# Optimization experiments

Measured on AMD Instinct MI355X. Metric: run time of the kernel, lower is better.

Reference implementation:

```python
import jax, jax.numpy as jnp
import numpy as np

FEATS = 1024
HEAD = 16
MLP_HIDDEN = 4096
B, N = 8, 1024
EPS = 1e-5


def _layernorm(x, g, b):
    mu = jnp.mean(x, axis=-1, keepdims=True)
    var = jnp.var(x, axis=-1, keepdims=True)
    return (x - mu) * jax.lax.rsqrt(var + EPS) * g + b


def setup_inputs() -> dict:
    key = jax.random.key(0)
    ks = jax.random.split(key, 12)
    s_attn = 1.0 / np.sqrt(FEATS)
    s_mlp1 = 1.0 / np.sqrt(FEATS)
    s_mlp2 = 1.0 / np.sqrt(MLP_HIDDEN)
    return {
        "x": jax.random.normal(ks[0], (B, N, FEATS), dtype=jnp.float32),
        "ln1_g": jnp.ones((FEATS,), jnp.float32),
        "ln1_b": jnp.zeros((FEATS,), jnp.float32),
        "wq": jax.random.normal(ks[1], (FEATS, FEATS), jnp.float32) * s_attn,
        "bq": jnp.zeros((FEATS,), jnp.float32),
        "wk": jax.random.normal(ks[2], (FEATS, FEATS), jnp.float32) * s_attn,
        "bk": jnp.zeros((FEATS,), jnp.float32),
        "wv": jax.random.normal(ks[3], (FEATS, FEATS), jnp.float32) * s_attn,
        "bv": jnp.zeros((FEATS,), jnp.float32),
        "wo": jax.random.normal(ks[4], (FEATS, FEATS), jnp.float32) * s_attn,
        "bo": jnp.zeros((FEATS,), jnp.float32),
        "ln2_g": jnp.ones((FEATS,), jnp.float32),
        "ln2_b": jnp.zeros((FEATS,), jnp.float32),
        "w1": jax.random.normal(ks[5], (FEATS, MLP_HIDDEN), jnp.float32) * s_mlp1,
        "b1": jnp.zeros((MLP_HIDDEN,), jnp.float32),
        "w2": jax.random.normal(ks[6], (MLP_HIDDEN, FEATS), jnp.float32) * s_mlp2,
        "b2": jnp.zeros((FEATS,), jnp.float32),
    }


def reference(x, ln1_g, ln1_b, wq, bq, wk, bk, wv, bv, wo, bo,
              ln2_g, ln2_b, w1, b1, w2, b2):
    b, n, f = x.shape
    d = f // HEAD
    sqrt_d = jnp.asarray(f, x.dtype) ** 0.5  # NOTE: scale by sqrt(feats), as in source

    h = _layernorm(x, ln1_g, ln1_b)
    # [b, n, f] -> [b, head, n, d]
    q = (h @ wq + bq).reshape(b, n, HEAD, d).transpose(0, 2, 1, 3)
    k = (h @ wk + bk).reshape(b, n, HEAD, d).transpose(0, 2, 1, 3)
    v = (h @ wv + bv).reshape(b, n, HEAD, d).transpose(0, 2, 1, 3)

    score = jnp.einsum('bhif,bhjf->bhij', q, k) / sqrt_d
    p = jax.nn.softmax(score, axis=-1)
    attn = jnp.einsum('bhij,bhjf->bihf', p, v).reshape(b, n, f)
    o = attn @ wo + bo
    out = o + x

    h2 = _layernorm(out, ln2_g, ln2_b)
    m = jax.nn.gelu(h2 @ w1 + b1, approximate=False)
    m = jax.nn.gelu(m @ w2 + b2, approximate=False)
    return m + out
```

## Files before the change

kernel.cpp:

```cpp
#include <hip/hip_runtime.h>
#include <cstdint>

typedef __bf16 bf16;
typedef __attribute__((ext_vector_type(8))) __bf16 bf16x8;
typedef __attribute__((ext_vector_type(4))) __bf16 bf16x4;
typedef __attribute__((ext_vector_type(4))) float f32x4;
typedef __attribute__((ext_vector_type(8))) unsigned short u16x8;

#define AS1C(p) ((const __attribute__((address_space(1))) void*)(p))
#define AS3(p)  ((__attribute__((address_space(3))) void*)(p))

__device__ __forceinline__ float gelu_exact(float v) {
    return 0.5f * v * (1.0f + erff(v * 0.7071067811865476f));
}

__global__ __launch_bounds__(256, 1) void wtrans_kernel(
    const float* __restrict__ w, bf16* __restrict__ wt, int K, int N)
{
    __shared__ float tile[64][65];
    const int k0 = blockIdx.y * 64, n0 = blockIdx.x * 64;
    const int tid = threadIdx.x;
    {
        const int kl = tid >> 2, nc = (tid & 3) * 16;
        #pragma unroll
        for (int i = 0; i < 4; ++i) {
            const float4 v = *(const float4*)&w[(size_t)(k0 + kl) * N + n0 + nc + i * 4];
            tile[kl][nc + i * 4 + 0] = v.x;
            tile[kl][nc + i * 4 + 1] = v.y;
            tile[kl][nc + i * 4 + 2] = v.z;
            tile[kl][nc + i * 4 + 3] = v.w;
        }
    }
    __syncthreads();
    {
        const int nl = tid >> 2, kc = (tid & 3) * 16;
        #pragma unroll
        for (int i = 0; i < 4; ++i) {
            bf16x4 o4;
            o4[0] = (bf16)tile[kc + i * 4 + 0][nl];
            o4[1] = (bf16)tile[kc + i * 4 + 1][nl];
            o4[2] = (bf16)tile[kc + i * 4 + 2][nl];
            o4[3] = (bf16)tile[kc + i * 4 + 3][nl];
            *(bf16x4*)&wt[(size_t)(n0 + nl) * K + k0 + kc + i * 4] = o4;
        }
    }
}

__global__ void bias3_kernel(const float* __restrict__ a, const float* __restrict__ b,
                             const float* __restrict__ c, float* __restrict__ o)
{
    const int i = blockIdx.x * 256 + threadIdx.x;
    o[i] = (i < 1024) ? a[i] : (i < 2048 ? b[i - 1024] : c[i - 2048]);
}

__global__ __launch_bounds__(256, 1) void ln_kernel(
    const float* __restrict__ x, const float* __restrict__ gw,
    const float* __restrict__ bw, bf16* __restrict__ out)
{
    const int row = blockIdx.x, tid = threadIdx.x;
    const float4 v = *(const float4*)&x[(size_t)row * 1024 + tid * 4];
    float s = v.x + v.y + v.z + v.w;
    float q = v.x * v.x + v.y * v.y + v.z * v.z + v.w * v.w;
    #pragma unroll
    for (int off = 32; off > 0; off >>= 1) {
        s += __shfl_xor(s, off);
        q += __shfl_xor(q, off);
    }
    __shared__ float red[8];
    if ((tid & 63) == 0) { red[tid >> 6] = s; red[4 + (tid >> 6)] = q; }
    __syncthreads();
    s = red[0] + red[1] + red[2] + red[3];
    q = red[4] + red[5] + red[6] + red[7];
    const float mu = s * (1.f / 1024.f);
    const float rs = rsqrtf(q * (1.f / 1024.f) - mu * mu + 1e-5f);
    const float4 gg = *(const float4*)&gw[tid * 4];
    const float4 bb = *(const float4*)&bw[tid * 4];
    bf16x4 o4;
    o4[0] = (bf16)((v.x - mu) * rs * gg.x + bb.x);
    o4[1] = (bf16)((v.y - mu) * rs * gg.y + bb.y);
    o4[2] = (bf16)((v.z - mu) * rs * gg.z + bb.z);
    o4[3] = (bf16)((v.w - mu) * rs * gg.w + bb.w);
    *(bf16x4*)&out[(size_t)row * 1024 + tid * 4] = o4;
}

template<int EPI>
__global__ __launch_bounds__(512, 2) void gemm_v7_kernel(
    const bf16* __restrict__ A, const bf16* __restrict__ BT,
    const float* __restrict__ bias, const float* __restrict__ res,
    void* __restrict__ out, int M, int N, int K)
{
    constexpr int ABYTES = 256 * 128;
    constexpr int BUFB = 384 * 128;
    extern __shared__ char lds[];

    const int tid = threadIdx.x;
    const int lane = tid & 63, wid = tid >> 6;
    const int wr = wid >> 1, wc = wid & 1;
    const int j = lane & 15, g = lane >> 4;
    const int skc = ((tid & 7) ^ ((tid >> 4) & 7)) << 3;

    const int nbn = N >> 7;
    const int nwg = (M >> 8) * nbn;
    const int bid = blockIdx.x;
    const int wg = (bid & 7) * (nwg >> 3) + (bid >> 3);
    const int bm = (wg / nbn) << 8;
    const int bn = (wg % nbn) << 7;

    auto stage = [&](int k0, char* obuf) {
        #pragma unroll
        for (int ga = 0; ga < 4; ++ga) {
            const bf16* src = A + (size_t)(bm + ga * 64 + (tid >> 3)) * K + k0 + skc;
            __builtin_amdgcn_global_load_lds(AS1C(src), AS3(obuf + ga * 8192 + tid * 16), 16, 0, 0);
        }
        #pragma unroll
        for (int gb = 0; gb < 2; ++gb) {
            const bf16* src = BT + (size_t)(bn + gb * 64 + (tid >> 3)) * K + k0 + skc;
            __builtin_amdgcn_global_load_lds(AS1C(src), AS3(obuf + ABYTES + gb * 8192 + tid * 16), 16, 0, 0);
        }
    };

    f32x4 acc[4][4] = {};
    const int NT = K >> 6;

    stage(0, lds);
    stage(64, lds + BUFB);
    asm volatile("s_waitcnt vmcnt(6)" ::: "memory");
    __builtin_amdgcn_s_barrier();

    int cur = 0;
    for (int t = 0; t < NT; ++t) {
        char* buf = lds + cur * BUFB;
        const int nxt2 = (cur >= 1) ? cur - 1 : 2;

        bf16x8 af[4][2], bfr[2][2];
        #pragma unroll
        for (int mf = 0; mf < 4; ++mf)
            #pragma unroll
            for (int ks = 0; ks < 2; ++ks) {
                const int R = wr * 64 + mf * 16 + j;
                uint32_t lb = (uint32_t)(R * 128 + ks * 64 + g * 16);
                lb ^= (lb >> 4) & 0x70u;
                af[mf][ks] = *(const bf16x8*)(buf + lb);
            }
        #pragma unroll
        for (int nf = 0; nf < 2; ++nf)
            #pragma unroll
            for (int ks = 0; ks < 2; ++ks) {
                const int R = wc * 64 + nf * 16 + j;
                uint32_t lb = (uint32_t)(R * 128 + ks * 64 + g * 16);
                lb ^= (lb >> 4) & 0x70u;
                bfr[nf][ks] = *(const bf16x8*)(buf + ABYTES + lb);
            }
        if (t + 2 < NT) stage((t + 2) << 6, lds + nxt2 * BUFB);
        __builtin_amdgcn_s_barrier();
        asm volatile("s_waitcnt lgkmcnt(0)" ::: "memory");
        __builtin_amdgcn_sched_barrier(0);
        __builtin_amdgcn_s_setprio(1);
        #pragma unroll
        for (int mf = 0; mf < 4; ++mf)
            #pragma unroll
            for (int nf = 0; nf < 2; ++nf)
                #pragma unroll
                for (int ks = 0; ks < 2; ++ks)
                    acc[mf][nf] = __builtin_amdgcn_mfma_f32_16x16x32_bf16(
                        af[mf][ks], bfr[nf][ks], acc[mf][nf], 0, 0, 0);
        __builtin_amdgcn_s_setprio(0);
        __builtin_amdgcn_s_barrier();

        bf16x8 bfr2[2][2];
        #pragma unroll
        for (int nf = 0; nf < 2; ++nf)
            #pragma unroll
            for (int ks = 0; ks < 2; ++ks) {
                const int R = wc * 64 + (2 + nf) * 16 + j;
                uint32_t lb = (uint32_t)(R * 128 + ks * 64 + g * 16);
                lb ^= (lb >> 4) & 0x70u;
                bfr2[nf][ks] = *(const bf16x8*)(buf + ABYTES + lb);
            }
        __builtin_amdgcn_s_barrier();
        asm volatile("s_waitcnt lgkmcnt(0)" ::: "memory");
        __builtin_amdgcn_sched_barrier(0);
        __builtin_amdgcn_s_setprio(1);
        #pragma unroll
        for (int mf = 0; mf < 4; ++mf)
            #pragma unroll
            for (int nf = 0; nf < 2; ++nf)
                #pragma unroll
                for (int ks = 0; ks < 2; ++ks)
                    acc[mf][2 + nf] = __builtin_amdgcn_mfma_f32_16x16x32_bf16(
                        af[mf][ks], bfr2[nf][ks], acc[mf][2 + nf], 0, 0, 0);
        __builtin_amdgcn_s_setprio(0);
        if (t + 2 < NT) asm volatile("s_waitcnt vmcnt(6)" ::: "memory");
        else            asm volatile("s_waitcnt vmcnt(0)" ::: "memory");
        __builtin_amdgcn_s_barrier();

        cur = (cur == 2) ? 0 : cur + 1;
    }

    const int row0 = bm + wr * 64;
    const int col0 = bn + wc * 64;
    #pragma unroll
    for (int nf = 0; nf < 4; ++nf) {
        const int col = col0 + nf * 16 + j;
        const float bs = bias[col];
        #pragma unroll
        for (int mf = 0; mf < 4; ++mf) {
            #pragma unroll
            for (int r = 0; r < 4; ++r) {
                const int row = row0 + mf * 16 + g * 4 + r;
                float v = acc[mf][nf][r] + bs;
                if constexpr (EPI == 2 || EPI == 3) v = gelu_exact(v);
                if constexpr (EPI == 1 || EPI == 3) {
                    v += res[(size_t)row * N + col];
                    ((float*)out)[(size_t)row * N + col] = v;
                } else {
                    ((bf16*)out)[(size_t)row * N + col] = (bf16)v;
                }
            }
        }
    }
}

__global__ __launch_bounds__(256, 1) void attn_kernel(
    const bf16* __restrict__ qkv, bf16* __restrict__ attn, int bh_base)
{
    const int tid = threadIdx.x;
    const int lane = tid & 63, wid = tid >> 6;
    const int j = lane & 15, g = lane >> 4;

    const int lin = blockIdx.x + blockIdx.y * 8;
    const int virt = (lin & 7) * 64 + (lin >> 3);
    const int bh = bh_base + (virt >> 3), qp = virt & 7;
    const int b = bh >> 4, h = bh & 15;
    const int q0a = qp * 128 + wid * 16;
    const int q0b = q0a + 64;

    const bf16* Qp = qkv + (size_t)b * 1024 * 3072 + h * 64;
    const bf16* Kp = Qp + 1024;
    const bf16* Vp = Qp + 2048;

    __shared__ __attribute__((aligned(16))) uint32_t vTu[4][64][36];

    const int kp = (tid & 31) * 2;
    const int d0 = (tid >> 5) * 8;
    #pragma unroll
    for (int pb = 0; pb < 2; ++pb) {
        const u16x8 r0 = *(const u16x8*)&Vp[(size_t)(pb * 64 + kp) * 3072 + d0];
        const u16x8 r1 = *(const u16x8*)&Vp[(size_t)(pb * 64 + kp + 1) * 3072 + d0];
        #pragma unroll
        for (int i = 0; i < 8; ++i)
            vTu[pb][d0 + i][kp >> 1] = (uint32_t)r0[i] | ((uint32_t)r1[i] << 16);
    }

    bf16x8 qa0 = *(const bf16x8*)&Qp[(size_t)(q0a + j) * 3072 + g * 8];
    bf16x8 qa1 = *(const bf16x8*)&Qp[(size_t)(q0a + j) * 3072 + 32 + g * 8];
    bf16x8 qb0 = *(const bf16x8*)&Qp[(size_t)(q0b + j) * 3072 + g * 8];
    bf16x8 qb1 = *(const bf16x8*)&Qp[(size_t)(q0b + j) * 3072 + 32 + g * 8];
    #pragma unroll
    for (int e = 0; e < 8; ++e) {
        qa0[e] = (bf16)((float)qa0[e] * 0.03125f);
        qa1[e] = (bf16)((float)qa1[e] * 0.03125f);
        qb0[e] = (bf16)((float)qb0[e] * 0.03125f);
        qb1[e] = (bf16)((float)qb1[e] * 0.03125f);
    }

    const int jperm = (j >> 2) * 8 + (j & 3);

    f32x4 oa[4] = {}, ob[4] = {};
    float mra = -1e30f, lsa = 0.f;
    float mrb = -1e30f, lsb = 0.f;

    bf16x8 kfA[4][2], kfB[4][2];
    #pragma unroll
    for (int t = 0; t < 4; ++t) {
        const int key = (t >> 1) * 32 + jperm + (t & 1) * 4;
        kfA[t][0] = *(const bf16x8*)&Kp[(size_t)key * 3072 + g * 8];
        kfA[t][1] = *(const bf16x8*)&Kp[(size_t)key * 3072 + 32 + g * 8];
    }

    asm volatile("s_waitcnt lgkmcnt(0)" ::: "memory");
    __builtin_amdgcn_s_barrier();

    auto softmax = [&](f32x4 (&s)[4], float& mrun, float& lsum, f32x4 (&o)[4]) {
        float cur = fmaxf(fmaxf(s[0][0], s[0][1]), fmaxf(s[0][2], s[0][3]));
        #pragma unroll
        for (int t = 1; t < 4; ++t)
            cur = fmaxf(cur, fmaxf(fmaxf(s[t][0], s[t][1]), fmaxf(s[t][2], s[t][3])));
        cur = fmaxf(cur, __shfl_xor(cur, 16));
        cur = fmaxf(cur, __shfl_xor(cur, 32));
        if (!__all(cur - mrun <= 8.0f)) {
            const float mnew = fmaxf(mrun, cur);
            const float alpha = __expf(mrun - mnew);
            float al[4];
            #pragma unroll
            for (int r = 0; r < 4; ++r) al[r] = __shfl(alpha, g * 4 + r);
            #pragma unroll
            for (int dt = 0; dt < 4; ++dt)
                #pragma unroll
                for (int r = 0; r < 4; ++r) o[dt][r] *= al[r];
            lsum *= alpha;
            mrun = mnew;
        }
        float ps = 0.f;
        #pragma unroll
        for (int t = 0; t < 4; ++t)
            #pragma unroll
            for (int r = 0; r < 4; ++r) {
                const float p = __expf(s[t][r] - mrun);
                s[t][r] = p;
                ps += p;
            }
        lsum += ps;
    };

    auto iter = [&](int c, bf16x8 (&kf)[4][2], bf16x8 (&kfn)[4][2]) {
        const f32x4 zero = {0.f, 0.f, 0.f, 0.f};
        const bool pfv = (c + 2 < 16);
        const bool pfk = (c + 1 < 16);

        u16x8 r0, r1;
        if (pfv) {
            const size_t vb = (size_t)((c + 2) * 64 + kp) * 3072 + d0;
            r0 = *(const u16x8*)&Vp[vb];
            r1 = *(const u16x8*)&Vp[vb + 3072];
        }

        f32x4 sa[4], sb[4];
        #pragma unroll
        for (int t = 0; t < 4; ++t) {
            sa[t] = __builtin_amdgcn_mfma_f32_16x16x32_bf16(kf[t][0], qa0, zero, 0, 0, 0);
            sb[t] = __builtin_amdgcn_mfma_f32_16x16x32_bf16(kf[t][0], qb0, zero, 0, 0, 0);
            sa[t] = __builtin_amdgcn_mfma_f32_16x16x32_bf16(kf[t][1], qa1, sa[t], 0, 0, 0);
            sb[t] = __builtin_amdgcn_mfma_f32_16x16x32_bf16(kf[t][1], qb1, sb[t], 0, 0, 0);
        }

        if (pfk) {
            #pragma unroll
            for (int t = 0; t < 4; ++t) {
                const int key = (c + 1) * 64 + (t >> 1) * 32 + jperm + (t & 1) * 4;
                kfn[t][0] = *(const bf16x8*)&Kp[(size_t)key * 3072 + g * 8];
                kfn[t][1] = *(const bf16x8*)&Kp[(size_t)key * 3072 + 32 + g * 8];
            }
        }

        softmax(sa, mra, lsa, oa);
        softmax(sb, mrb, lsb, ob);

        bf16x8 paa0, paa1, pab0, pab1;
        #pragma unroll
        for (int r = 0; r < 4; ++r) {
            paa0[r]     = (bf16)sa[0][r];
            paa0[4 + r] = (bf16)sa[1][r];
            paa1[r]     = (bf16)sa[2][r];
            paa1[4 + r] = (bf16)sa[3][r];
            pab0[r]     = (bf16)sb[0][r];
            pab0[4 + r] = (bf16)sb[1][r];
            pab1[r]     = (bf16)sb[2][r];
            pab1[4 + r] = (bf16)sb[3][r];
        }

        if (pfv) {
            const int wb = (c + 2) & 3;
            #pragma unroll
            for (int i = 0; i < 8; ++i)
                vTu[wb][d0 + i][kp >> 1] = (uint32_t)r0[i] | ((uint32_t)r1[i] << 16);
        }

        const int rb = c & 3;
        #pragma unroll
        for (int dt = 0; dt < 4; ++dt) {
            const bf16* vrow = (const bf16*)&vTu[rb][dt * 16 + j][0];
            const bf16x8 vb0 = *(const bf16x8*)(vrow + g * 8);
            const bf16x8 vb1 = *(const bf16x8*)(vrow + 32 + g * 8);
            oa[dt] = __builtin_amdgcn_mfma_f32_16x16x32_bf16(paa0, vb0, oa[dt], 0, 0, 0);
            ob[dt] = __builtin_amdgcn_mfma_f32_16x16x32_bf16(pab0, vb0, ob[dt], 0, 0, 0);
            oa[dt] = __builtin_amdgcn_mfma_f32_16x16x32_bf16(paa1, vb1, oa[dt], 0, 0, 0);
            ob[dt] = __builtin_amdgcn_mfma_f32_16x16x32_bf16(pab1, vb1, ob[dt], 0, 0, 0);
        }
    };

    for (int cc = 0; cc < 16; cc += 2) {
        iter(cc,     kfA, kfB);
        iter(cc + 1, kfB, kfA);
        asm volatile("s_waitcnt lgkmcnt(0)" ::: "memory");
        __builtin_amdgcn_sched_barrier(0);
        __builtin_amdgcn_s_barrier();
    }

    lsa += __shfl_xor(lsa, 16);
    lsa += __shfl_xor(lsa, 32);
    lsb += __shfl_xor(lsb, 16);
    lsb += __shfl_xor(lsb, 32);
    float inva[4], invb[4];
    #pragma unroll
    for (int r = 0; r < 4; ++r) {
        inva[r] = 1.0f / __shfl(lsa, g * 4 + r);
        invb[r] = 1.0f / __shfl(lsb, g * 4 + r);
    }
    #pragma unroll
    for (int dt = 0; dt < 4; ++dt)
        #pragma unroll
        for (int r = 0; r < 4; ++r) {
            attn[(size_t)(b * 1024 + q0a + g * 4 + r) * 1024 + h * 64 + dt * 16 + j] =
                (bf16)(oa[dt][r] * inva[r]);
            attn[(size_t)(b * 1024 + q0b + g * 4 + r) * 1024 + h * 64 + dt * 16 + j] =
                (bf16)(ob[dt][r] * invb[r]);
        }
}

extern "C" void kernel_launch(void* const* d_in, const int* in_sizes, int n_in,
                              void* d_out, int out_size, void* d_ws, size_t ws_size,
                              hipStream_t stream)
{
    const float* x    = (const float*)d_in[0];
    const float* ln1g = (const float*)d_in[1];
    const float* ln1b = (const float*)d_in[2];
    const float* wq   = (const float*)d_in[3];
    const float* bq   = (const float*)d_in[4];
    const float* wk   = (const float*)d_in[5];
    const float* bk   = (const float*)d_in[6];
    const float* wv   = (const float*)d_in[7];
    const float* bv   = (const float*)d_in[8];
    const float* wo   = (const float*)d_in[9];
    const float* bo   = (const float*)d_in[10];
    const float* ln2g = (const float*)d_in[11];
    const float* ln2b = (const float*)d_in[12];
    const float* w1   = (const float*)d_in[13];
    const float* b1   = (const float*)d_in[14];
    const float* w2   = (const float*)d_in[15];
    const float* b2   = (const float*)d_in[16];

    char* ws = (char*)d_ws;
    bf16* wqkvT = (bf16*)ws;  ws += (size_t)3072 * 1024 * 2;
    bf16* woT   = (bf16*)ws;  ws += (size_t)1024 * 1024 * 2;
    bf16* w1T   = (bf16*)ws;  ws += (size_t)4096 * 1024 * 2;
    bf16* w2T   = (bf16*)ws;  ws += (size_t)1024 * 4096 * 2;
    float* bqkv = (float*)ws; ws += (size_t)3072 * 4;
    bf16* h     = (bf16*)ws;  ws += (size_t)8192 * 1024 * 2;
    bf16* qkv   = (bf16*)ws;  ws += (size_t)8192 * 3072 * 2;
    bf16* attn  = (bf16*)ws;  ws += (size_t)8192 * 1024 * 2;
    float* outf = (float*)ws; ws += (size_t)8192 * 1024 * 4;
    bf16* m1    = (bf16*)ws;  ws += (size_t)8192 * 4096 * 2;

    (void)hipFuncSetAttribute((const void*)gemm_v7_kernel<0>,
                              hipFuncAttributeMaxDynamicSharedMemorySize, 147456);
    (void)hipFuncSetAttribute((const void*)gemm_v7_kernel<1>,
                              hipFuncAttributeMaxDynamicSharedMemorySize, 147456);
    (void)hipFuncSetAttribute((const void*)gemm_v7_kernel<2>,
                              hipFuncAttributeMaxDynamicSharedMemorySize, 147456);
    (void)hipFuncSetAttribute((const void*)gemm_v7_kernel<3>,
                              hipFuncAttributeMaxDynamicSharedMemorySize, 147456);

    wtrans_kernel<<<dim3(16, 16), 256, 0, stream>>>(wq, wqkvT,                   1024, 1024);
    wtrans_kernel<<<dim3(16, 16), 256, 0, stream>>>(wk, wqkvT + 1024 * 1024,     1024, 1024);
    wtrans_kernel<<<dim3(16, 16), 256, 0, stream>>>(wv, wqkvT + 2 * 1024 * 1024, 1024, 1024);
    wtrans_kernel<<<dim3(16, 16), 256, 0, stream>>>(wo, woT, 1024, 1024);
    wtrans_kernel<<<dim3(64, 16), 256, 0, stream>>>(w1, w1T, 1024, 4096);
    wtrans_kernel<<<dim3(16, 64), 256, 0, stream>>>(w2, w2T, 4096, 1024);
    bias3_kernel<<<12, 256, 0, stream>>>(bq, bk, bv, bqkv);

    ln_kernel<<<8192, 256, 0, stream>>>(x, ln1g, ln1b, h);
    gemm_v7_kernel<0><<<768, 512, 147456, stream>>>(h, wqkvT, bqkv, nullptr, qkv, 8192, 3072, 1024);
    attn_kernel<<<dim3(8, 64), 256, 0, stream>>>(qkv, attn, 0);
    attn_kernel<<<dim3(8, 64), 256, 0, stream>>>(qkv, attn, 64);
    gemm_v7_kernel<1><<<256, 512, 147456, stream>>>(attn, woT, bo, x, outf, 8192, 1024, 1024);
    ln_kernel<<<8192, 256, 0, stream>>>(outf, ln2g, ln2b, h);
    gemm_v7_kernel<2><<<1024, 512, 147456, stream>>>(h, w1T, b1, nullptr, m1, 8192, 4096, 1024);
    gemm_v7_kernel<3><<<256, 512, 147456, stream>>>(m1, w2T, b2, outf, (float*)d_out, 8192, 1024, 4096);
}
```

Before: 449.9 us.

## Enlarge GEMM tiles to 256x256, double-buffer, and split-K the final MLP GEMM

The GEMM moves from 256x128 tiles with a three-stage buffer to 256x256 tiles with a two-stage double buffer. Each wave now computes a 128x64 sub-tile, which raises MFMA work per LDS read. The down-projection GEMM is split in two along K, writing fp32 partial sums, and a new reduce kernel adds them with bias, GELU and the residual. Larger tiles halve the number of workgroups, so the grid may underfill the CUs. The shallower pipeline and full vmcnt(0) waits expose more memory latency, and split-K adds extra fp32 traffic.

```diff
diff --git a/kernel.cpp b/kernel.cpp
--- a/kernel.cpp
+++ b/kernel.cpp
@@ -84,133 +84,135 @@
 }
 
 template<int EPI>
-__global__ __launch_bounds__(512, 2) void gemm_v7_kernel(
+__global__ __launch_bounds__(512, 2) void gemm_v10_kernel(
     const bf16* __restrict__ A, const bf16* __restrict__ BT,
     const float* __restrict__ bias, const float* __restrict__ res,
-    void* __restrict__ out, int M, int N, int K)
+    void* __restrict__ out, int M, int N, int Kstride, int Klen)
 {
     constexpr int ABYTES = 256 * 128;
-    constexpr int BUFB = 384 * 128;
+    constexpr int BUFB = 512 * 128;
     extern __shared__ char lds[];
 
     const int tid = threadIdx.x;
     const int lane = tid & 63, wid = tid >> 6;
-    const int wr = wid >> 1, wc = wid & 1;
+    const int wr = wid >> 2, wc = wid & 3;
     const int j = lane & 15, g = lane >> 4;
     const int skc = ((tid & 7) ^ ((tid >> 4) & 7)) << 3;
 
-    const int nbn = N >> 7;
+    const int nbn = N >> 8;
     const int nwg = (M >> 8) * nbn;
-    const int bid = blockIdx.x;
-    const int wg = (bid & 7) * (nwg >> 3) + (bid >> 3);
-    const int bm = (wg / nbn) << 8;
-    const int bn = (wg % nbn) << 7;
-
-    auto stage = [&](int k0, char* obuf) {
+    const int wg = (blockIdx.x & 7) * ((int)gridDim.x >> 3) + (blockIdx.x >> 3);
+    const int half = wg / nwg;
+    const int wgl = wg - half * nwg;
+    const int bm = (wgl / nbn) << 8;
+    const int bn = (wgl % nbn) << 8;
+    const int kbase = half * Klen;
+
+    const bf16* srcA[4];
+    const bf16* srcB[4];
+    #pragma unroll
+    for (int ga = 0; ga < 4; ++ga)
+        srcA[ga] = A + (size_t)(bm + ga * 64 + (tid >> 3)) * Kstride + kbase + skc;
+    #pragma unroll
+    for (int gb = 0; gb < 4; ++gb)
+        srcB[gb] = BT + (size_t)(bn + gb * 64 + (tid >> 3)) * Kstride + kbase + skc;
+
+    auto stage = [&](char* obuf) {
         #pragma unroll
         for (int ga = 0; ga < 4; ++ga) {
-            const bf16* src = A + (size_t)(bm + ga * 64 + (tid >> 3)) * K + k0 + skc;
-            __builtin_amdgcn_global_load_lds(AS1C(src), AS3(obuf + ga * 8192 + tid * 16), 16, 0, 0);
-        }
-        #pragma unroll
-        for (int gb = 0; gb < 2; ++gb) {
-            const bf16* src = BT + (size_t)(bn + gb * 64 + (tid >> 3)) * K + k0 + skc;
-            __builtin_amdgcn_global_load_lds(AS1C(src), AS3(obuf + ABYTES + gb * 8192 + tid * 16), 16, 0, 0);
+            __builtin_amdgcn_global_load_lds(AS1C(srcA[ga]), AS3(obuf + ga * 8192 + tid * 16), 16, 0, 0);
+            srcA[ga] += 64;
+        }
+        #pragma unroll
+        for (int gb = 0; gb < 4; ++gb) {
+            __builtin_amdgcn_global_load_lds(AS1C(srcB[gb]), AS3(obuf + ABYTES + gb * 8192 + tid * 16), 16, 0, 0);
+            srcB[gb] += 64;
         }
     };
-
-    f32x4 acc[4][4] = {};
-    const int NT = K >> 6;
-
-    stage(0, lds);
-    stage(64, lds + BUFB);
-    asm volatile("s_waitcnt vmcnt(6)" ::: "memory");
+    auto rdA = [&](char* buf, int h, int mf, int ks) {
+        const int R = wr * 128 + (h * 4 + mf) * 16 + j;
+        uint32_t lb = (uint32_t)(R * 128 + ks * 64 + g * 16);
+        lb ^= (lb >> 4) & 0x70u;
+        return *(const bf16x8*)(buf + lb);
+    };
+    auto rdB = [&](char* buf, int nf, int ks) {
+        const int R = wc * 64 + nf * 16 + j;
+        uint32_t lb = (uint32_t)(R * 128 + ks * 64 + g * 16);
+        lb ^= (lb >> 4) & 0x70u;
+        return *(const bf16x8*)(buf + ABYTES + lb);
+    };
+
+    f32x4 acc[8][4] = {};
+    const int NT = Klen >> 6;
+
+    stage(lds);
+    asm volatile("s_waitcnt vmcnt(0)" ::: "memory");
     __builtin_amdgcn_s_barrier();
 
-    int cur = 0;
     for (int t = 0; t < NT; ++t) {
-        char* buf = lds + cur * BUFB;
-        const int nxt2 = (cur >= 1) ? cur - 1 : 2;
-
-        bf16x8 af[4][2], bfr[2][2];
+        char* buf = lds + (t & 1) * BUFB;
+
+        bf16x8 bfr[4][2], af[4][2];
+        #pragma unroll
+        for (int nf = 0; nf < 4; ++nf)
+            #pragma unroll
+            for (int ks = 0; ks < 2; ++ks) bfr[nf][ks] = rdB(buf, nf, ks);
         #pragma unroll
         for (int mf = 0; mf < 4; ++mf)
             #pragma unroll
-            for (int ks = 0; ks < 2; ++ks) {
-                const int R = wr * 64 + mf * 16 + j;
-                uint32_t lb = (uint32_t)(R * 128 + ks * 64 + g * 16);
-                lb ^= (lb >> 4) & 0x70u;
-                af[mf][ks] = *(const bf16x8*)(buf + lb);
-            }
-        #pragma unroll
-        for (int nf = 0; nf < 2; ++nf)
-            #pragma unroll
-            for (int ks = 0; ks < 2; ++ks) {
-                const int R = wc * 64 + nf * 16 + j;
-                uint32_t lb = (uint32_t)(R * 128 + ks * 64 + g * 16);
-                lb ^= (lb >> 4) & 0x70u;
-                bfr[nf][ks] = *(const bf16x8*)(buf + ABYTES + lb);
-            }
-        if (t + 2 < NT) stage((t + 2) << 6, lds + nxt2 * BUFB);
-        __builtin_amdgcn_s_barrier();
-        asm volatile("s_waitcnt lgkmcnt(0)" ::: "memory");
+            for (int ks = 0; ks < 2; ++ks) af[mf][ks] = rdA(buf, 0, mf, ks);
+        if (t + 1 < NT) stage(lds + ((t + 1) & 1) * BUFB);
         __builtin_amdgcn_sched_barrier(0);
         __builtin_amdgcn_s_setprio(1);
         #pragma unroll
         for (int mf = 0; mf < 4; ++mf)
             #pragma unroll
-            for (int nf = 0; nf < 2; ++nf)
+            for (int nf = 0; nf < 4; ++nf)
                 #pragma unroll
                 for (int ks = 0; ks < 2; ++ks)
                     acc[mf][nf] = __builtin_amdgcn_mfma_f32_16x16x32_bf16(
                         af[mf][ks], bfr[nf][ks], acc[mf][nf], 0, 0, 0);
         __builtin_amdgcn_s_setprio(0);
-        __builtin_amdgcn_s_barrier();
-
-        bf16x8 bfr2[2][2];
-        #pragma unroll
-        for (int nf = 0; nf < 2; ++nf)
-            #pragma unroll
-            for (int ks = 0; ks < 2; ++ks) {
-                const int R = wc * 64 + (2 + nf) * 16 + j;
-                uint32_t lb = (uint32_t)(R * 128 + ks * 64 + g * 16);
-                lb ^= (lb >> 4) & 0x70u;
-                bfr2[nf][ks] = *(const bf16x8*)(buf + ABYTES + lb);
-            }
-        __builtin_amdgcn_s_barrier();
-        asm volatile("s_waitcnt lgkmcnt(0)" ::: "memory");
+        bf16x8 af1[4][2];
+        #pragma unroll
+        for (int mf = 0; mf < 4; ++mf)
+            #pragma unroll
+            for (int ks = 0; ks < 2; ++ks) af1[mf][ks] = rdA(buf, 1, mf, ks);
         __builtin_amdgcn_sched_barrier(0);
         __builtin_amdgcn_s_setprio(1);
         #pragma unroll
         for (int mf = 0; mf < 4; ++mf)
             #pragma unroll
-            for (int nf = 0; nf < 2; ++nf)
+            for (int nf = 0; nf < 4; ++nf)
                 #pragma unroll
                 for (int ks = 0; ks < 2; ++ks)
-                    acc[mf][2 + nf] = __builtin_amdgcn_mfma_f32_16x16x32_bf16(
-                        af[mf][ks], bfr2[nf][ks], acc[mf][2 + nf], 0, 0, 0);
+                    acc[4 + mf][nf] = __builtin_amdgcn_mfma_f32_16x16x32_bf16(
+                        af1[mf][ks], bfr[nf][ks], acc[4 + mf][nf], 0, 0, 0);
         __builtin_amdgcn_s_setprio(0);
-        if (t + 2 < NT) asm volatile("s_waitcnt vmcnt(6)" ::: "memory");
-        else            asm volatile("s_waitcnt vmcnt(0)" ::: "memory");
+        asm volatile("s_waitcnt vmcnt(0)" ::: "memory");
         __builtin_amdgcn_s_barrier();
-
-        cur = (cur == 2) ? 0 : cur + 1;
-    }
-
-    const int row0 = bm + wr * 64;
+    }
+
+    const int row0 = bm + wr * 128;
     const int col0 = bn + wc * 64;
+    float* po = nullptr;
+    if constexpr (EPI == 4)
+        po = half ? (float*)res : (float*)out;
     #pragma unroll
     for (int nf = 0; nf < 4; ++nf) {
         const int col = col0 + nf * 16 + j;
-        const float bs = bias[col];
-        #pragma unroll
-        for (int mf = 0; mf < 4; ++mf) {
+        const float bs = (EPI == 4) ? 0.f : bias[col];
+        #pragma unroll
+        for (int mf = 0; mf < 8; ++mf) {
             #pragma unroll
             for (int r = 0; r < 4; ++r) {
                 const int row = row0 + mf * 16 + g * 4 + r;
                 float v = acc[mf][nf][r] + bs;
-                if constexpr (EPI == 2 || EPI == 3) v = gelu_exact(v);
-                if constexpr (EPI == 1 || EPI == 3) {
+                if constexpr (EPI == 4) {
+                    po[(size_t)row * N + col] = v;
+                } else if constexpr (EPI == 2) {
+                    ((bf16*)out)[(size_t)row * N + col] = (bf16)gelu_exact(v);
+                } else if constexpr (EPI == 1) {
                     v += res[(size_t)row * N + col];
                     ((float*)out)[(size_t)row * N + col] = v;
                 } else {
@@ -219,6 +221,24 @@
             }
         }
     }
+}
+
+__global__ __launch_bounds__(256, 1) void reduce2_kernel(
+    const float* __restrict__ p0, const float* __restrict__ p1,
+    const float* __restrict__ bias, const float* __restrict__ res,
+    float* __restrict__ out)
+{
+    const size_t i4 = ((size_t)blockIdx.x * 256 + threadIdx.x) * 4;
+    const float4 a = *(const float4*)&p0[i4];
+    const float4 b = *(const float4*)&p1[i4];
+    const float4 r = *(const float4*)&res[i4];
+    const float4 bs = *(const float4*)&bias[i4 & 1023];
+    float4 o;
+    o.x = gelu_exact(a.x + b.x + bs.x) + r.x;
+    o.y = gelu_exact(a.y + b.y + bs.y) + r.y;
+    o.z = gelu_exact(a.z + b.z + bs.z) + r.z;
+    o.w = gelu_exact(a.w + b.w + bs.w) + r.w;
+    *(float4*)&out[i4] = o;
 }
 
 __global__ __launch_bounds__(256, 1) void attn_kernel(
@@ -441,15 +461,17 @@
     bf16* attn  = (bf16*)ws;  ws += (size_t)8192 * 1024 * 2;
     float* outf = (float*)ws; ws += (size_t)8192 * 1024 * 4;
     bf16* m1    = (bf16*)ws;  ws += (size_t)8192 * 4096 * 2;
-
-    (void)hipFuncSetAttribute((const void*)gemm_v7_kernel<0>,
-                              hipFuncAttributeMaxDynamicSharedMemorySize, 147456);
-    (void)hipFuncSetAttribute((const void*)gemm_v7_kernel<1>,
-                              hipFuncAttributeMaxDynamicSharedMemorySize, 147456);
-    (void)hipFuncSetAttribute((const void*)gemm_v7_kernel<2>,
-                              hipFuncAttributeMaxDynamicSharedMemorySize, 147456);
-    (void)hipFuncSetAttribute((const void*)gemm_v7_kernel<3>,
-                              hipFuncAttributeMaxDynamicSharedMemorySize, 147456);
+    float* p1   = (float*)ws; ws += (size_t)8192 * 1024 * 4;
+    float* p0   = (float*)qkv;
+
+    (void)hipFuncSetAttribute((const void*)gemm_v10_kernel<0>,
+                              hipFuncAttributeMaxDynamicSharedMemorySize, 131072);
+    (void)hipFuncSetAttribute((const void*)gemm_v10_kernel<1>,
+                              hipFuncAttributeMaxDynamicSharedMemorySize, 131072);
+    (void)hipFuncSetAttribute((const void*)gemm_v10_kernel<2>,
+                              hipFuncAttributeMaxDynamicSharedMemorySize, 131072);
+    (void)hipFuncSetAttribute((const void*)gemm_v10_kernel<4>,
+                              hipFuncAttributeMaxDynamicSharedMemorySize, 131072);
 
     wtrans_kernel<<<dim3(16, 16), 256, 0, stream>>>(wq, wqkvT,                   1024, 1024);
     wtrans_kernel<<<dim3(16, 16), 256, 0, stream>>>(wk, wqkvT + 1024 * 1024,     1024, 1024);
@@ -460,11 +482,12 @@
     bias3_kernel<<<12, 256, 0, stream>>>(bq, bk, bv, bqkv);
 
     ln_kernel<<<8192, 256, 0, stream>>>(x, ln1g, ln1b, h);
-    gemm_v7_kernel<0><<<768, 512, 147456, stream>>>(h, wqkvT, bqkv, nullptr, qkv, 8192, 3072, 1024);
+    gemm_v10_kernel<0><<<384, 512, 131072, stream>>>(h, wqkvT, bqkv, nullptr, qkv, 8192, 3072, 1024, 1024);
     attn_kernel<<<dim3(8, 64), 256, 0, stream>>>(qkv, attn, 0);
     attn_kernel<<<dim3(8, 64), 256, 0, stream>>>(qkv, attn, 64);
-    gemm_v7_kernel<1><<<256, 512, 147456, stream>>>(attn, woT, bo, x, outf, 8192, 1024, 1024);
+    gemm_v10_kernel<1><<<128, 512, 131072, stream>>>(attn, woT, bo, x, outf, 8192, 1024, 1024, 1024);
     ln_kernel<<<8192, 256, 0, stream>>>(outf, ln2g, ln2b, h);
-    gemm_v7_kernel<2><<<1024, 512, 147456, stream>>>(h, w1T, b1, nullptr, m1, 8192, 4096, 1024);
-    gemm_v7_kernel<3><<<256, 512, 147456, stream>>>(m1, w2T, b2, outf, (float*)d_out, 8192, 1024, 4096);
-}
+    gemm_v10_kernel<2><<<512, 512, 131072, stream>>>(h, w1T, b1, nullptr, m1, 8192, 4096, 1024, 1024);
+    gemm_v10_kernel<4><<<256, 512, 131072, stream>>>(m1, w2T, nullptr, p1, p0, 8192, 1024, 4096, 2048);
+    reduce2_kernel<<<8192, 256, 0, stream>>>(p0, p1, b2, outf, (float*)d_out);
+}
```

After: 449.4 us (median of 3 runs). About the same (-0.1%).

## Add 256x256-tile double-buffered GEMM for MLP up-projection and merge attention launches

Applied to the files above, without the earlier changes.

Adds a new GEMM kernel with 256x256 output tiles, a 64-wide K step, XOR-swizzled LDS and double-buffered direct global-to-LDS loads. It interleaves MFMA work with LDS reads under setprio, and the GELU up-projection GEMM now runs on it with 512 workgroups. The two half-size attention launches are merged into one launch covering all batch-heads, which removes a launch and the tail between them. The larger tiles raise data reuse per workgroup but need 128 KB of LDS and many accumulator registers per thread, which may limit occupancy.

```diff
diff --git a/kernel.cpp b/kernel.cpp
--- a/kernel.cpp
+++ b/kernel.cpp
@@ -221,16 +221,151 @@
     }
 }
 
+template<int EPI>
+__global__ __launch_bounds__(512, 2) void gemm_v10_kernel(
+    const bf16* __restrict__ A, const bf16* __restrict__ BT,
+    const float* __restrict__ bias, const float* __restrict__ res,
+    void* __restrict__ out, int M, int N, int Kstride, int Klen)
+{
+    constexpr int ABYTES = 256 * 128;
+    constexpr int BUFB = 512 * 128;
+    extern __shared__ char lds[];
+
+    const int tid = threadIdx.x;
+    const int lane = tid & 63, wid = tid >> 6;
+    const int wr = wid >> 2, wc = wid & 3;
+    const int j = lane & 15, g = lane >> 4;
+    const int skc = ((tid & 7) ^ ((tid >> 4) & 7)) << 3;
+
+    const int nbn = N >> 8;
+    const int nwg = (M >> 8) * nbn;
+    const int wg = (blockIdx.x & 7) * ((int)gridDim.x >> 3) + (blockIdx.x >> 3);
+    const int half = wg / nwg;
+    const int wgl = wg - half * nwg;
+    const int bm = (wgl / nbn) << 8;
+    const int bn = (wgl % nbn) << 8;
+    const int kbase = half * Klen;
+
+    const bf16* srcA[4];
+    const bf16* srcB[4];
+    #pragma unroll
+    for (int ga = 0; ga < 4; ++ga)
+        srcA[ga] = A + (size_t)(bm + ga * 64 + (tid >> 3)) * Kstride + kbase + skc;
+    #pragma unroll
+    for (int gb = 0; gb < 4; ++gb)
+        srcB[gb] = BT + (size_t)(bn + gb * 64 + (tid >> 3)) * Kstride + kbase + skc;
+
+    auto stage = [&](char* obuf) {
+        #pragma unroll
+        for (int ga = 0; ga < 4; ++ga) {
+            __builtin_amdgcn_global_load_lds(AS1C(srcA[ga]), AS3(obuf + ga * 8192 + tid * 16), 16, 0, 0);
+            srcA[ga] += 64;
+        }
+        #pragma unroll
+        for (int gb = 0; gb < 4; ++gb) {
+            __builtin_amdgcn_global_load_lds(AS1C(srcB[gb]), AS3(obuf + ABYTES + gb * 8192 + tid * 16), 16, 0, 0);
+            srcB[gb] += 64;
+        }
+    };
+    auto rdA = [&](char* buf, int h, int mf, int ks) {
+        const int R = wr * 128 + (h * 4 + mf) * 16 + j;
+        uint32_t lb = (uint32_t)(R * 128 + ks * 64 + g * 16);
+        lb ^= (lb >> 4) & 0x70u;
+        return *(const bf16x8*)(buf + lb);
+    };
+    auto rdB = [&](char* buf, int nf, int ks) {
+        const int R = wc * 64 + nf * 16 + j;
+        uint32_t lb = (uint32_t)(R * 128 + ks * 64 + g * 16);
+        lb ^= (lb >> 4) & 0x70u;
+        return *(const bf16x8*)(buf + ABYTES + lb);
+    };
+
+    f32x4 acc[8][4] = {};
+    const int NT = Klen >> 6;
+
+    stage(lds);
+    asm volatile("s_waitcnt vmcnt(0)" ::: "memory");
+    __builtin_amdgcn_s_barrier();
+
+    for (int t = 0; t < NT; ++t) {
+        char* buf = lds + (t & 1) * BUFB;
+
+        bf16x8 bfr[4][2], af[4][2];
+        #pragma unroll
+        for (int nf = 0; nf < 4; ++nf)
+            #pragma unroll
+            for (int ks = 0; ks < 2; ++ks) bfr[nf][ks] = rdB(buf, nf, ks);
+        #pragma unroll
+        for (int mf = 0; mf < 4; ++mf)
+            #pragma unroll
+            for (int ks = 0; ks < 2; ++ks) af[mf][ks] = rdA(buf, 0, mf, ks);
+        if (t + 1 < NT) stage(lds + ((t + 1) & 1) * BUFB);
+        __builtin_amdgcn_sched_barrier(0);
+        __builtin_amdgcn_s_setprio(1);
+        #pragma unroll
+        for (int mf = 0; mf < 4; ++mf)
+            #pragma unroll
+            for (int nf = 0; nf < 4; ++nf)
+                #pragma unroll
+                for (int ks = 0; ks < 2; ++ks)
+                    acc[mf][nf] = __builtin_amdgcn_mfma_f32_16x16x32_bf16(
+                        af[mf][ks], bfr[nf][ks], acc[mf][nf], 0, 0, 0);
+        __builtin_amdgcn_s_setprio(0);
+        bf16x8 af1[4][2];
+        #pragma unroll
+        for (int mf = 0; mf < 4; ++mf)
+            #pragma unroll
+            for (int ks = 0; ks < 2; ++ks) af1[mf][ks] = rdA(buf, 1, mf, ks);
+        __builtin_amdgcn_sched_barrier(0);
+        __builtin_amdgcn_s_setprio(1);
+        #pragma unroll
+        for (int mf = 0; mf < 4; ++mf)
+            #pragma unroll
+            for (int nf = 0; nf < 4; ++nf)
+                #pragma unroll
+                for (int ks = 0; ks < 2; ++ks)
+                    acc[4 + mf][nf] = __builtin_amdgcn_mfma_f32_16x16x32_bf16(
+                        af1[mf][ks], bfr[nf][ks], acc[4 + mf][nf], 0, 0, 0);
+        __builtin_amdgcn_s_setprio(0);
+        asm volatile("s_waitcnt vmcnt(0)" ::: "memory");
+        __builtin_amdgcn_s_barrier();
+    }
+
+    const int row0 = bm + wr * 128;
+    const int col0 = bn + wc * 64;
+    #pragma unroll
+    for (int nf = 0; nf < 4; ++nf) {
+        const int col = col0 + nf * 16 + j;
+        const float bs = bias[col];
+        #pragma unroll
+        for (int mf = 0; mf < 8; ++mf) {
+            #pragma unroll
+            for (int r = 0; r < 4; ++r) {
+                const int row = row0 + mf * 16 + g * 4 + r;
+                float v = acc[mf][nf][r] + bs;
+                if constexpr (EPI == 2) {
+                    ((bf16*)out)[(size_t)row * N + col] = (bf16)gelu_exact(v);
+                } else if constexpr (EPI == 1) {
+                    v += res[(size_t)row * N + col];
+                    ((float*)out)[(size_t)row * N + col] = v;
+                } else {
+                    ((bf16*)out)[(size_t)row * N + col] = (bf16)v;
+                }
+            }
+        }
+    }
+}
+
 __global__ __launch_bounds__(256, 1) void attn_kernel(
-    const bf16* __restrict__ qkv, bf16* __restrict__ attn, int bh_base)
+    const bf16* __restrict__ qkv, bf16* __restrict__ attn)
 {
     const int tid = threadIdx.x;
     const int lane = tid & 63, wid = tid >> 6;
     const int j = lane & 15, g = lane >> 4;
 
     const int lin = blockIdx.x + blockIdx.y * 8;
-    const int virt = (lin & 7) * 64 + (lin >> 3);
-    const int bh = bh_base + (virt >> 3), qp = virt & 7;
+    const int virt = (lin & 7) * 128 + (lin >> 3);
+    const int bh = virt >> 3, qp = virt & 7;
     const int b = bh >> 4, h = bh & 15;
     const int q0a = qp * 128 + wid * 16;
     const int q0b = q0a + 64;
@@ -446,10 +581,10 @@
                               hipFuncAttributeMaxDynamicSharedMemorySize, 147456);
     (void)hipFuncSetAttribute((const void*)gemm_v7_kernel<1>,
                               hipFuncAttributeMaxDynamicSharedMemorySize, 147456);
-    (void)hipFuncSetAttribute((const void*)gemm_v7_kernel<2>,
-                              hipFuncAttributeMaxDynamicSharedMemorySize, 147456);
     (void)hipFuncSetAttribute((const void*)gemm_v7_kernel<3>,
                               hipFuncAttributeMaxDynamicSharedMemorySize, 147456);
+    (void)hipFuncSetAttribute((const void*)gemm_v10_kernel<2>,
+                              hipFuncAttributeMaxDynamicSharedMemorySize, 131072);
 
     wtrans_kernel<<<dim3(16, 16), 256, 0, stream>>>(wq, wqkvT,                   1024, 1024);
     wtrans_kernel<<<dim3(16, 16), 256, 0, stream>>>(wk, wqkvT + 1024 * 1024,     1024, 1024);
@@ -461,10 +596,9 @@
 
     ln_kernel<<<8192, 256, 0, stream>>>(x, ln1g, ln1b, h);
     gemm_v7_kernel<0><<<768, 512, 147456, stream>>>(h, wqkvT, bqkv, nullptr, qkv, 8192, 3072, 1024);
-    attn_kernel<<<dim3(8, 64), 256, 0, stream>>>(qkv, attn, 0);
-    attn_kernel<<<dim3(8, 64), 256, 0, stream>>>(qkv, attn, 64);
+    attn_kernel<<<dim3(8, 128), 256, 0, stream>>>(qkv, attn);
     gemm_v7_kernel<1><<<256, 512, 147456, stream>>>(attn, woT, bo, x, outf, 8192, 1024, 1024);
     ln_kernel<<<8192, 256, 0, stream>>>(outf, ln2g, ln2b, h);
-    gemm_v7_kernel<2><<<1024, 512, 147456, stream>>>(h, w1T, b1, nullptr, m1, 8192, 4096, 1024);
+    gemm_v10_kernel<2><<<512, 512, 131072, stream>>>(h, w1T, b1, nullptr, m1, 8192, 4096, 1024, 1024);
     gemm_v7_kernel<3><<<256, 512, 147456, stream>>>(m1, w2T, b2, outf, (float*)d_out, 8192, 1024, 4096);
 }
```

Measured after the change: 454.8 us. About the same (+1.1%).
